# Performance work log

Hardware: AMD Instinct MI355X
Metric: run time of the kernel (lower is better)

Reference implementation:

```python
import jax, jax.numpy as jnp
import numpy as np

B, S, N, H, NH = 2, 2048, 1024, 1024, 16
D = H // NH  # head dim = 64


def setup_inputs() -> dict:
    key = jax.random.key(0)
    ks = jax.random.split(key, 7)
    scale = 1.0 / np.sqrt(H)
    return {
        "token_q": jax.random.normal(ks[0], (B, S, H), dtype=jnp.float32),
        "block_kv": jax.random.normal(ks[1], (B, N, H), dtype=jnp.float32),
        "block_ends": jnp.sort(jax.random.randint(ks[2], (N,), 0, S, dtype=jnp.int32)),
        "Wq": jax.random.normal(ks[3], (H, H), dtype=jnp.float32) * scale,
        "Wk": jax.random.normal(ks[4], (H, H), dtype=jnp.float32) * scale,
        "Wv": jax.random.normal(ks[5], (H, H), dtype=jnp.float32) * scale,
        "Wo": jax.random.normal(ks[6], (H, H), dtype=jnp.float32) * scale,
    }


def reference(token_q, block_kv, block_ends, Wq, Wk, Wv, Wo):
    # nn.Linear: y = x @ W.T (no bias)
    q = (token_q @ Wq.T).reshape(B, S, NH, D).transpose(0, 2, 1, 3)   # [B,h,S,d]
    k = (block_kv @ Wk.T).reshape(B, N, NH, D).transpose(0, 2, 1, 3)  # [B,h,N,d]
    v = (block_kv @ Wv.T).reshape(B, N, NH, D).transpose(0, 2, 1, 3)  # [B,h,N,d]

    attn = jnp.einsum("bhsd,bhnd->bhsn", q, k) / jnp.sqrt(jnp.float32(D))

    # strict_causal mask: block is visible iff its end position <= query index t
    t_idx = jnp.arange(S, dtype=block_ends.dtype)[:, None]           # [S,1]
    mask = block_ends[None, :] <= t_idx                               # [S,N]
    neg = jnp.finfo(attn.dtype).min
    attn = jnp.where(mask[None, None, :, :], attn, neg)

    attn = jax.nn.softmax(attn, axis=-1)
    out = jnp.einsum("bhsn,bhnd->bhsd", attn, v)                      # [B,h,S,d]
    out = out.transpose(0, 2, 1, 3).reshape(B, S, H)
    return out @ Wo.T
```

## Files before the change

### kernel.cpp

```cpp
#include <hip/hip_runtime.h>
#include <float.h>
#include <stdint.h>

#define B_  2
#define S_  2048
#define N_  1024
#define H_  1024
#define NH_ 16
#define K_  1024

typedef __attribute__((ext_vector_type(8))) short bf16x8;
typedef __attribute__((ext_vector_type(4))) float f32x4;

typedef __attribute__((address_space(3))) uint32_t lds_u32;
typedef __attribute__((address_space(1))) uint32_t glb_u32;

__device__ __forceinline__ void gload16(void* l, const void* g) {
    __builtin_amdgcn_global_load_lds((const glb_u32*)g, (lds_u32*)l, 16, 0, 0);
}

__device__ __forceinline__ ushort f2bf(float f) {
    uint32_t u = __float_as_uint(f);
    u = (u + 0x7fffu + ((u >> 16) & 1u)) >> 16;
    return (ushort)u;
}

#if __has_builtin(__builtin_amdgcn_cvt_pk_bf16_f32)
typedef __attribute__((ext_vector_type(2))) __bf16 bfp2;
__device__ __forceinline__ uint pk2(float a, float b) {
    bfp2 v = __builtin_amdgcn_cvt_pk_bf16_f32(a, b);
    return __builtin_bit_cast(uint, v);
}
#else
__device__ __forceinline__ uint pk2(float a, float b) {
    return (uint)f2bf(a) | ((uint)f2bf(b) << 16);
}
#endif

__device__ __forceinline__ float fexp2(float x) {
#if __has_builtin(__builtin_amdgcn_exp2f)
    return __builtin_amdgcn_exp2f(x);
#else
    return exp2f(x);
#endif
}

#define SC2 0.180336880f

__global__ __launch_bounds__(256) void prep_kernel(const float* __restrict__ tq,
        const float* __restrict__ kv, const float* __restrict__ wq,
        const float* __restrict__ wk, const float* __restrict__ wv,
        const float* __restrict__ wo, const int* __restrict__ ends,
        ushort* __restrict__ dst, int* __restrict__ cnt, float* __restrict__ Vm)
{
    int blk = blockIdx.x;
    if (blk >= 5120) {
        if (blk == 5128) {
            float4 z = make_float4(0.f, 0.f, 0.f, 0.f);
            *(float4*)(Vm + threadIdx.x * 8) = z;
            *(float4*)(Vm + threadIdx.x * 8 + 4) = z;
            return;
        }
        int t = (blk - 5120) * 256 + threadIdx.x;
        if (t < S_) {
            int lo = 0, hi = N_;
            while (lo < hi) { int mid = (lo + hi) >> 1; if (ends[mid] <= t) lo = mid + 1; else hi = mid; }
            cnt[t] = lo;
        }
        return;
    }
    const float* src; size_t base;
    if (blk < 2048)      { src = tq; base = 0;       }
    else if (blk < 3072) { src = kv; base = 4194304; blk -= 2048; }
    else if (blk < 3584) { src = wq; base = 6291456; blk -= 3072; }
    else if (blk < 4096) { src = wk; base = 7340032; blk -= 3584; }
    else if (blk < 4608) { src = wv; base = 8388608; blk -= 4096; }
    else                 { src = wo; base = 9437184; blk -= 4608; }
    size_t i = (size_t)blk * 2048 + threadIdx.x * 8;
    float4 a = *(const float4*)(src + i);
    float4 b = *(const float4*)(src + i + 4);
    uint4 o;
    o.x = pk2(a.x, a.y); o.y = pk2(a.z, a.w);
    o.z = pk2(b.x, b.y); o.w = pk2(b.z, b.w);
    *(uint4*)(dst + base + i) = o;
}

__global__ __launch_bounds__(512) void gemm_all(int mode,
        const ushort* __restrict__ qx, const ushort* __restrict__ kvx,
        const ushort* __restrict__ wq, const ushort* __restrict__ wk,
        const ushort* __restrict__ wv, const ushort* __restrict__ wo,
        ushort* __restrict__ Qp, ushort* __restrict__ Kp,
        ushort* __restrict__ VtG, const ushort* __restrict__ AO,
        float* __restrict__ outF, float* __restrict__ Vm)
{
    __shared__ __align__(16) ushort smem[17408];
    ushort* Xs = smem;
    ushort* Ws = smem + 8192;

    const ushort* X; const ushort* W; void* Yp; int kind; float scale = 1.f;
    int bm, bn;
    if (mode == 1) {
        X = AO; W = wo; Yp = outF; kind = 1;
        bm = (blockIdx.x >> 3) * 128; bn = (blockIdx.x & 7) * 128;
    } else {
        int idx = blockIdx.x;
        if (idx < 256)      { X = qx;  W = wq; Yp = Qp;  kind = 0; scale = SC2;
                              bm = (idx >> 3) * 128; bn = (idx & 7) * 128; }
        else if (idx < 384) { int j = idx - 256; X = kvx; W = wk; Yp = Kp; kind = 0;
                              bm = (j >> 3) * 128; bn = (j & 7) * 128; }
        else                { int j = idx - 384; X = kvx; W = wv; Yp = VtG; kind = 2;
                              bm = (j >> 3) * 128; bn = (j & 7) * 128; }
    }

    const int tid = threadIdx.x;
    const int lane = tid & 63, w = tid >> 6;
    const int wy = w >> 1, wx = w & 1;
    const int c = lane & 15, g = lane >> 4;

    f32x4 acc[2][4] = {};

    for (int kt = 0; kt < 16; ++kt) {
        const int k0 = kt * 64;
#pragma unroll
        for (int j = 0; j < 2; ++j) {
            int u = w * 128 + j * 64 + lane;
            int row = u >> 3, gs = (u & 7) ^ (row & 7);
            gload16(Xs + (w * 128 + j * 64) * 8, X + (size_t)(bm + row) * K_ + k0 + gs * 8);
            gload16(Ws + (w * 128 + j * 64) * 8, W + (size_t)(bn + row) * K_ + k0 + gs * 8);
        }
        __syncthreads();
#pragma unroll
        for (int ks = 0; ks < 2; ++ks) {
            bf16x8 af[2], bfr[4];
#pragma unroll
            for (int mi = 0; mi < 2; ++mi) {
                int row = wy * 32 + mi * 16 + c;
                int s = ks * 4 + g;
                af[mi] = *(const bf16x8*)(Xs + (row * 8 + (s ^ (row & 7))) * 8);
            }
#pragma unroll
            for (int ni = 0; ni < 4; ++ni) {
                int row = wx * 64 + ni * 16 + c;
                int s = ks * 4 + g;
                bfr[ni] = *(const bf16x8*)(Ws + (row * 8 + (s ^ (row & 7))) * 8);
            }
#pragma unroll
            for (int mi = 0; mi < 2; ++mi)
#pragma unroll
                for (int ni = 0; ni < 4; ++ni)
                    acc[mi][ni] = __builtin_amdgcn_mfma_f32_16x16x32_bf16(af[mi], bfr[ni], acc[mi][ni], 0, 0, 0);
        }
        __syncthreads();
    }

    if (kind == 0) {
        ushort* Y = (ushort*)Yp;
#pragma unroll
        for (int mi = 0; mi < 2; ++mi)
#pragma unroll
            for (int ni = 0; ni < 4; ++ni)
#pragma unroll
                for (int r = 0; r < 4; ++r) {
                    int row = bm + wy * 32 + mi * 16 + g * 4 + r;
                    int col = bn + wx * 64 + ni * 16 + c;
                    Y[(size_t)row * 1024 + col] = f2bf(acc[mi][ni][r] * scale);
                }
    } else if (kind == 1) {
        float* Y = (float*)Yp;
#pragma unroll
        for (int mi = 0; mi < 2; ++mi)
#pragma unroll
            for (int ni = 0; ni < 4; ++ni)
#pragma unroll
                for (int r = 0; r < 4; ++r) {
                    int row = bm + wy * 32 + mi * 16 + g * 4 + r;
                    int col = bn + wx * 64 + ni * 16 + c;
                    Y[(size_t)row * 1024 + col] = acc[mi][ni][r];
                }
    } else {
        ushort* T = smem;
#pragma unroll
        for (int mi = 0; mi < 2; ++mi)
#pragma unroll
            for (int ni = 0; ni < 4; ++ni) {
                ushort4 v4;
                v4.x = f2bf(acc[mi][ni][0]); v4.y = f2bf(acc[mi][ni][1]);
                v4.z = f2bf(acc[mi][ni][2]); v4.w = f2bf(acc[mi][ni][3]);
                *(ushort4*)&T[(wx * 64 + ni * 16 + c) * 136 + wy * 32 + mi * 16 + g * 4] = v4;
            }
        __syncthreads();
        ushort* Vt = (ushort*)Yp;
        int b = bm >> 10;
        int rid = tid >> 2, quad = tid & 3;
        int n_c = bn + rid;
        int h = n_c >> 6, d = n_c & 63;
        int m0 = quad * 32;
        ushort* dst = Vt + (size_t)((b * NH_ + h) * 64 + d) * N_ + (bm & (N_ - 1)) + m0;
        float vsum = 0.f;
#pragma unroll
        for (int jj = 0; jj < 4; ++jj) {
            uint4 tt = *(const uint4*)&T[rid * 136 + m0 + jj * 8];
            *(uint4*)(dst + jj * 8) = tt;
            uint uu[4] = {tt.x, tt.y, tt.z, tt.w};
#pragma unroll
            for (int q2 = 0; q2 < 4; ++q2) {
                vsum += __uint_as_float(uu[q2] << 16);
                vsum += __uint_as_float(uu[q2] & 0xffff0000u);
            }
        }
        vsum += __shfl_xor(vsum, 1);
        vsum += __shfl_xor(vsum, 2);
        if (quad == 0) atomicAdd(&Vm[b * 1024 + n_c], vsum);
    }
}

__global__ __launch_bounds__(256) void attn_mfma(const ushort* __restrict__ Qp,
                                                 const ushort* __restrict__ Kp,
                                                 const ushort* __restrict__ VtG,
                                                 const int* __restrict__ cnt,
                                                 const float* __restrict__ Vm,
                                                 ushort* __restrict__ AO)
{
    __shared__ __align__(16) ushort Qs[128 * 64];
    __shared__ __align__(16) ushort Ks[64 * 64];
    __shared__ __align__(16) ushort Vs[64 * 64];
    __shared__ __align__(16) ushort Ps[128][72];

    const int id = blockIdx.x;
    const int b = id & 1, h = (id >> 1) & 15;
    const int tb = id >> 5;
    const int t0 = (tb < 8 ? tb : 23 - tb) << 7;
    const int tid = threadIdx.x, lane = tid & 63, w = tid >> 6;
    const int c = lane & 15, g = lane >> 4;

#pragma unroll
    for (int jj = 0; jj < 4; ++jj) {
        int u = w * 256 + jj * 64 + lane;
        int row = u >> 3, gs = (u & 7) ^ (row & 7);
        gload16(Qs + (w * 256 + jj * 64) * 8,
                Qp + (size_t)(b * S_ + t0 + row) * H_ + h * 64 + gs * 8);
    }
    const int cntv0 = cnt[t0 + w * 32 + c];
    const int cntv1 = cnt[t0 + w * 32 + 16 + c];
    const int cnt_min = cnt[t0];
    const int ntmax = (cnt[t0 + 127] + 63) >> 6;

    const int u0 = (w * 2) * 64 + lane, row0 = u0 >> 3, gs0 = (u0 & 7) ^ (row0 & 7);
    const int u1 = (w * 2 + 1) * 64 + lane, row1 = u1 >> 3, gs1 = (u1 & 7) ^ (row1 & 7);
    const ushort* kp0 = Kp + (size_t)(b * N_ + row0) * H_ + h * 64 + gs0 * 8;
    const ushort* kp1 = Kp + (size_t)(b * N_ + row1) * H_ + h * 64 + gs1 * 8;
    const ushort* vp0 = VtG + (size_t)((b * NH_ + h) * 64 + row0) * N_ + gs0 * 8;
    const ushort* vp1 = VtG + (size_t)((b * NH_ + h) * 64 + row1) * N_ + gs1 * 8;

    float l0 = 0.f, l1 = 0.f;
    f32x4 o0[4] = {}, o1[4] = {};

    __syncthreads();
    bf16x8 bq0[2], bq1[2];
#pragma unroll
    for (int ks = 0; ks < 2; ++ks) {
        int s = ks * 4 + g;
        int ra = w * 32 + c;
        bq0[ks] = *(const bf16x8*)(Qs + (ra * 8 + (s ^ (ra & 7))) * 8);
        int rb = w * 32 + 16 + c;
        bq1[ks] = *(const bf16x8*)(Qs + (rb * 8 + (s ^ (rb & 7))) * 8);
    }

    for (int nt = 0; nt < ntmax; ++nt) {
        gload16(Ks + (w * 2) * 512, kp0 + (size_t)nt * 64 * H_);
        gload16(Ks + (w * 2 + 1) * 512, kp1 + (size_t)nt * 64 * H_);
        gload16(Vs + (w * 2) * 512, vp0 + nt * 64);
        gload16(Vs + (w * 2 + 1) * 512, vp1 + nt * 64);
        __syncthreads();

        f32x4 st0[4] = {}, st1[4] = {};
#pragma unroll
        for (int ntile = 0; ntile < 4; ++ntile)
#pragma unroll
            for (int ks = 0; ks < 2; ++ks) {
                int row = ntile * 16 + c;
                int s = ks * 4 + g;
                bf16x8 ak = *(const bf16x8*)(Ks + (row * 8 + (s ^ (row & 7))) * 8);
                st0[ntile] = __builtin_amdgcn_mfma_f32_16x16x32_bf16(ak, bq0[ks], st0[ntile], 0, 0, 0);
                st1[ntile] = __builtin_amdgcn_mfma_f32_16x16x32_bf16(ak, bq1[ks], st1[ntile], 0, 0, 0);
            }

        const bool full = ((nt + 1) << 6) <= cnt_min;
        float lsum0 = 0.f, lsum1 = 0.f;
        if (full) {
#pragma unroll
            for (int ntile = 0; ntile < 4; ++ntile) {
                float a0 = fexp2(st0[ntile][0]), a1 = fexp2(st0[ntile][1]);
                float a2 = fexp2(st0[ntile][2]), a3 = fexp2(st0[ntile][3]);
                lsum0 += (a0 + a1) + (a2 + a3);
                uint2 pw; pw.x = pk2(a0, a1); pw.y = pk2(a2, a3);
                *(uint2*)&Ps[w * 32 + c][ntile * 16 + g * 4] = pw;
                float b0 = fexp2(st1[ntile][0]), b1 = fexp2(st1[ntile][1]);
                float b2 = fexp2(st1[ntile][2]), b3 = fexp2(st1[ntile][3]);
                lsum1 += (b0 + b1) + (b2 + b3);
                uint2 qw; qw.x = pk2(b0, b1); qw.y = pk2(b2, b3);
                *(uint2*)&Ps[w * 32 + 16 + c][ntile * 16 + g * 4] = qw;
            }
        } else {
            const int base0 = (nt << 6) + g * 4 - cntv0;
            const int base1 = (nt << 6) + g * 4 - cntv1;
#pragma unroll
            for (int ntile = 0; ntile < 4; ++ntile) {
                float a0 = (base0 + ntile * 16 + 0 >= 0) ? 0.f : fexp2(st0[ntile][0]);
                float a1 = (base0 + ntile * 16 + 1 >= 0) ? 0.f : fexp2(st0[ntile][1]);
                float a2 = (base0 + ntile * 16 + 2 >= 0) ? 0.f : fexp2(st0[ntile][2]);
                float a3 = (base0 + ntile * 16 + 3 >= 0) ? 0.f : fexp2(st0[ntile][3]);
                lsum0 += (a0 + a1) + (a2 + a3);
                uint2 pw; pw.x = pk2(a0, a1); pw.y = pk2(a2, a3);
                *(uint2*)&Ps[w * 32 + c][ntile * 16 + g * 4] = pw;
                float b0 = (base1 + ntile * 16 + 0 >= 0) ? 0.f : fexp2(st1[ntile][0]);
                float b1 = (base1 + ntile * 16 + 1 >= 0) ? 0.f : fexp2(st1[ntile][1]);
                float b2 = (base1 + ntile * 16 + 2 >= 0) ? 0.f : fexp2(st1[ntile][2]);
                float b3 = (base1 + ntile * 16 + 3 >= 0) ? 0.f : fexp2(st1[ntile][3]);
                lsum1 += (b0 + b1) + (b2 + b3);
                uint2 qw; qw.x = pk2(b0, b1); qw.y = pk2(b2, b3);
                *(uint2*)&Ps[w * 32 + 16 + c][ntile * 16 + g * 4] = qw;
            }
        }
        lsum0 += __shfl_xor(lsum0, 16); lsum0 += __shfl_xor(lsum0, 32);
        lsum1 += __shfl_xor(lsum1, 16); lsum1 += __shfl_xor(lsum1, 32);
        l0 += lsum0; l1 += lsum1;

        bf16x8 ap0[2], ap1[2];
#pragma unroll
        for (int ks = 0; ks < 2; ++ks) {
            ap0[ks] = *(const bf16x8*)&Ps[w * 32 + c][ks * 32 + g * 8];
            ap1[ks] = *(const bf16x8*)&Ps[w * 32 + 16 + c][ks * 32 + g * 8];
        }
#pragma unroll
        for (int dt = 0; dt < 4; ++dt)
#pragma unroll
            for (int ks = 0; ks < 2; ++ks) {
                int row = dt * 16 + c;
                int s = ks * 4 + g;
                bf16x8 bv = *(const bf16x8*)(Vs + (row * 8 + (s ^ (row & 7))) * 8);
                o0[dt] = __builtin_amdgcn_mfma_f32_16x16x32_bf16(ap0[ks], bv, o0[dt], 0, 0, 0);
                o1[dt] = __builtin_amdgcn_mfma_f32_16x16x32_bf16(ap1[ks], bv, o1[dt], 0, 0, 0);
            }
        __syncthreads();
    }

#pragma unroll
    for (int qt = 0; qt < 2; ++qt) {
        float invl = 1.f / (qt == 0 ? l0 : l1);
        f32x4* o = (qt == 0 ? o0 : o1);
        float lr[4]; int cq[4];
#pragma unroll
        for (int r = 0; r < 4; ++r) {
            lr[r] = __shfl(invl, g * 4 + r);
            cq[r] = cnt[t0 + w * 32 + qt * 16 + g * 4 + r];
        }
#pragma unroll
        for (int dt = 0; dt < 4; ++dt)
#pragma unroll
            for (int r = 0; r < 4; ++r) {
                int q = t0 + w * 32 + qt * 16 + g * 4 + r;
                float val = o[dt][r] * lr[r];
                if (cq[r] == 0) val = Vm[b * 1024 + h * 64 + dt * 16 + c] * (1.f / 1024.f);
                AO[(size_t)(b * S_ + q) * H_ + h * 64 + dt * 16 + c] = f2bf(val);
            }
    }
}

extern "C" void kernel_launch(void* const* d_in, const int* in_sizes, int n_in,
                              void* d_out, int out_size, void* d_ws, size_t ws_size,
                              hipStream_t stream) {
    const float* token_q    = (const float*)d_in[0];
    const float* block_kv   = (const float*)d_in[1];
    const int*   block_ends = (const int*)d_in[2];
    const float* Wq = (const float*)d_in[3];
    const float* Wk = (const float*)d_in[4];
    const float* Wv = (const float*)d_in[5];
    const float* Wo = (const float*)d_in[6];
    float* out = (float*)d_out;

    ushort* ws  = (ushort*)d_ws;
    ushort* qx  = ws;
    ushort* kvx = ws + (size_t)4 * 1024 * 1024;
    ushort* wqb = ws + (size_t)6 * 1024 * 1024;
    ushort* wkb = ws + (size_t)7 * 1024 * 1024;
    ushort* wvb = ws + (size_t)8 * 1024 * 1024;
    ushort* wob = ws + (size_t)9 * 1024 * 1024;
    ushort* Qp  = ws + (size_t)10 * 1024 * 1024;
    ushort* Kp  = ws + (size_t)14 * 1024 * 1024;
    ushort* VtG = ws + (size_t)16 * 1024 * 1024;
    int*    cnt = (int*)(ws + (size_t)18 * 1024 * 1024);
    float*  Vm  = (float*)(ws + (size_t)18 * 1024 * 1024 + 4096);

    prep_kernel<<<5129, 256, 0, stream>>>(token_q, block_kv, Wq, Wk, Wv, Wo,
                                          block_ends, ws, cnt, Vm);
    gemm_all<<<512, 512, 0, stream>>>(0, qx, kvx, wqb, wkb, wvb, wob,
                                      Qp, Kp, VtG, nullptr, nullptr, Vm);
    attn_mfma<<<512, 256, 0, stream>>>(Qp, Kp, VtG, cnt, Vm, Qp);
    gemm_all<<<256, 512, 0, stream>>>(1, qx, kvx, wqb, wkb, wvb, wob,
                                      Qp, Kp, VtG, Qp, out, Vm);
}
```

Baseline: 163.0 us.

## Fuse fp32-to-bf16 conversion into GEMM loads and drop the prep kernel

```diff
diff --git a/kernel.cpp b/kernel.cpp
--- a/kernel.cpp
+++ b/kernel.cpp
@@ -47,68 +47,30 @@
 
 #define SC2 0.180336880f
 
-__global__ __launch_bounds__(256) void prep_kernel(const float* __restrict__ tq,
-        const float* __restrict__ kv, const float* __restrict__ wq,
-        const float* __restrict__ wk, const float* __restrict__ wv,
-        const float* __restrict__ wo, const int* __restrict__ ends,
-        ushort* __restrict__ dst, int* __restrict__ cnt, float* __restrict__ Vm)
-{
-    int blk = blockIdx.x;
-    if (blk >= 5120) {
-        if (blk == 5128) {
-            float4 z = make_float4(0.f, 0.f, 0.f, 0.f);
-            *(float4*)(Vm + threadIdx.x * 8) = z;
-            *(float4*)(Vm + threadIdx.x * 8 + 4) = z;
-            return;
-        }
-        int t = (blk - 5120) * 256 + threadIdx.x;
-        if (t < S_) {
-            int lo = 0, hi = N_;
-            while (lo < hi) { int mid = (lo + hi) >> 1; if (ends[mid] <= t) lo = mid + 1; else hi = mid; }
-            cnt[t] = lo;
-        }
-        return;
-    }
-    const float* src; size_t base;
-    if (blk < 2048)      { src = tq; base = 0;       }
-    else if (blk < 3072) { src = kv; base = 4194304; blk -= 2048; }
-    else if (blk < 3584) { src = wq; base = 6291456; blk -= 3072; }
-    else if (blk < 4096) { src = wk; base = 7340032; blk -= 3584; }
-    else if (blk < 4608) { src = wv; base = 8388608; blk -= 4096; }
-    else                 { src = wo; base = 9437184; blk -= 4608; }
-    size_t i = (size_t)blk * 2048 + threadIdx.x * 8;
-    float4 a = *(const float4*)(src + i);
-    float4 b = *(const float4*)(src + i + 4);
-    uint4 o;
-    o.x = pk2(a.x, a.y); o.y = pk2(a.z, a.w);
-    o.z = pk2(b.x, b.y); o.w = pk2(b.z, b.w);
-    *(uint4*)(dst + base + i) = o;
-}
-
 __global__ __launch_bounds__(512) void gemm_all(int mode,
-        const ushort* __restrict__ qx, const ushort* __restrict__ kvx,
-        const ushort* __restrict__ wq, const ushort* __restrict__ wk,
-        const ushort* __restrict__ wv, const ushort* __restrict__ wo,
+        const float* __restrict__ tqF, const float* __restrict__ kvF,
+        const float* __restrict__ wqF, const float* __restrict__ wkF,
+        const float* __restrict__ wvF, const float* __restrict__ woF,
         ushort* __restrict__ Qp, ushort* __restrict__ Kp,
         ushort* __restrict__ VtG, const ushort* __restrict__ AO,
-        float* __restrict__ outF, float* __restrict__ Vm)
+        float* __restrict__ outF, float* __restrict__ VmP)
 {
     __shared__ __align__(16) ushort smem[17408];
     ushort* Xs = smem;
     ushort* Ws = smem + 8192;
 
-    const ushort* X; const ushort* W; void* Yp; int kind; float scale = 1.f;
+    const float* XF = nullptr; const float* WF; void* Yp; int kind; float scale = 1.f;
     int bm, bn;
     if (mode == 1) {
-        X = AO; W = wo; Yp = outF; kind = 1;
+        WF = woF; Yp = outF; kind = 1;
         bm = (blockIdx.x >> 3) * 128; bn = (blockIdx.x & 7) * 128;
     } else {
         int idx = blockIdx.x;
-        if (idx < 256)      { X = qx;  W = wq; Yp = Qp;  kind = 0; scale = SC2;
+        if (idx < 256)      { XF = tqF; WF = wqF; Yp = Qp;  kind = 0; scale = SC2;
                               bm = (idx >> 3) * 128; bn = (idx & 7) * 128; }
-        else if (idx < 384) { int j = idx - 256; X = kvx; W = wk; Yp = Kp; kind = 0;
+        else if (idx < 384) { int j = idx - 256; XF = kvF; WF = wkF; Yp = Kp; kind = 0;
                               bm = (j >> 3) * 128; bn = (j & 7) * 128; }
-        else                { int j = idx - 384; X = kvx; W = wv; Yp = VtG; kind = 2;
+        else                { int j = idx - 384; XF = kvF; WF = wvF; Yp = VtG; kind = 2;
                               bm = (j >> 3) * 128; bn = (j & 7) * 128; }
     }
 
@@ -117,18 +79,63 @@
     const int wy = w >> 1, wx = w & 1;
     const int c = lane & 15, g = lane >> 4;
 
+    const int u0 = w * 128 + lane,      row0 = u0 >> 3, gs0 = (u0 & 7) ^ (row0 & 7);
+    const int u1 = w * 128 + 64 + lane, row1 = u1 >> 3, gs1 = (u1 & 7) ^ (row1 & 7);
+
+    const ushort* xb0 = nullptr; const ushort* xb1 = nullptr;
+    const float *xs0 = nullptr, *xs1 = nullptr;
+    if (mode == 1) {
+        xb0 = AO + (size_t)(bm + row0) * K_ + gs0 * 8;
+        xb1 = AO + (size_t)(bm + row1) * K_ + gs1 * 8;
+    } else {
+        xs0 = XF + (size_t)(bm + row0) * K_ + gs0 * 8;
+        xs1 = XF + (size_t)(bm + row1) * K_ + gs1 * 8;
+    }
+    const float* ws0 = WF + (size_t)(bn + row0) * K_ + gs0 * 8;
+    const float* ws1 = WF + (size_t)(bn + row1) * K_ + gs1 * 8;
+
+    float4 x0a, x0b, x1a, x1b, w0a, w0b, w1a, w1b;
+    uint4 bx0, bx1;
+
+    auto loadX = [&](int k0) {
+        if (mode == 1) {
+            bx0 = *(const uint4*)(xb0 + k0);
+            bx1 = *(const uint4*)(xb1 + k0);
+        } else {
+            x0a = *(const float4*)(xs0 + k0); x0b = *(const float4*)(xs0 + k0 + 4);
+            x1a = *(const float4*)(xs1 + k0); x1b = *(const float4*)(xs1 + k0 + 4);
+        }
+        w0a = *(const float4*)(ws0 + k0); w0b = *(const float4*)(ws0 + k0 + 4);
+        w1a = *(const float4*)(ws1 + k0); w1b = *(const float4*)(ws1 + k0 + 4);
+    };
+
     f32x4 acc[2][4] = {};
 
+    loadX(0);
     for (int kt = 0; kt < 16; ++kt) {
-        const int k0 = kt * 64;
-#pragma unroll
-        for (int j = 0; j < 2; ++j) {
-            int u = w * 128 + j * 64 + lane;
-            int row = u >> 3, gs = (u & 7) ^ (row & 7);
-            gload16(Xs + (w * 128 + j * 64) * 8, X + (size_t)(bm + row) * K_ + k0 + gs * 8);
-            gload16(Ws + (w * 128 + j * 64) * 8, W + (size_t)(bn + row) * K_ + k0 + gs * 8);
-        }
-        __syncthreads();
+        __syncthreads();
+        if (mode == 1) {
+            *(uint4*)(Xs + u0 * 8) = bx0;
+            *(uint4*)(Xs + u1 * 8) = bx1;
+        } else {
+            uint4 t0v = make_uint4(pk2(x0a.x, x0a.y), pk2(x0a.z, x0a.w),
+                                   pk2(x0b.x, x0b.y), pk2(x0b.z, x0b.w));
+            uint4 t1v = make_uint4(pk2(x1a.x, x1a.y), pk2(x1a.z, x1a.w),
+                                   pk2(x1b.x, x1b.y), pk2(x1b.z, x1b.w));
+            *(uint4*)(Xs + u0 * 8) = t0v;
+            *(uint4*)(Xs + u1 * 8) = t1v;
+        }
+        {
+            uint4 s0 = make_uint4(pk2(w0a.x, w0a.y), pk2(w0a.z, w0a.w),
+                                  pk2(w0b.x, w0b.y), pk2(w0b.z, w0b.w));
+            uint4 s1 = make_uint4(pk2(w1a.x, w1a.y), pk2(w1a.z, w1a.w),
+                                  pk2(w1b.x, w1b.y), pk2(w1b.z, w1b.w));
+            *(uint4*)(Ws + u0 * 8) = s0;
+            *(uint4*)(Ws + u1 * 8) = s1;
+        }
+        __syncthreads();
+        if (kt < 15) loadX((kt + 1) * 64);
+
 #pragma unroll
         for (int ks = 0; ks < 2; ++ks) {
             bf16x8 af[2], bfr[4];
@@ -150,7 +157,6 @@
                 for (int ni = 0; ni < 4; ++ni)
                     acc[mi][ni] = __builtin_amdgcn_mfma_f32_16x16x32_bf16(af[mi], bfr[ni], acc[mi][ni], 0, 0, 0);
         }
-        __syncthreads();
     }
 
     if (kind == 0) {
@@ -179,6 +185,7 @@
                 }
     } else {
         ushort* T = smem;
+        __syncthreads();
 #pragma unroll
         for (int mi = 0; mi < 2; ++mi)
 #pragma unroll
@@ -210,21 +217,22 @@
         }
         vsum += __shfl_xor(vsum, 1);
         vsum += __shfl_xor(vsum, 2);
-        if (quad == 0) atomicAdd(&Vm[b * 1024 + n_c], vsum);
+        if (quad == 0) VmP[(bm >> 7) * 1024 + n_c] = vsum;
     }
 }
 
 __global__ __launch_bounds__(256) void attn_mfma(const ushort* __restrict__ Qp,
                                                  const ushort* __restrict__ Kp,
                                                  const ushort* __restrict__ VtG,
-                                                 const int* __restrict__ cnt,
-                                                 const float* __restrict__ Vm,
+                                                 const int* __restrict__ ends,
+                                                 const float* __restrict__ VmP,
                                                  ushort* __restrict__ AO)
 {
     __shared__ __align__(16) ushort Qs[128 * 64];
     __shared__ __align__(16) ushort Ks[64 * 64];
     __shared__ __align__(16) ushort Vs[64 * 64];
     __shared__ __align__(16) ushort Ps[128][72];
+    __shared__ int cntS[128];
 
     const int id = blockIdx.x;
     const int b = id & 1, h = (id >> 1) & 15;
@@ -240,10 +248,12 @@
         gload16(Qs + (w * 256 + jj * 64) * 8,
                 Qp + (size_t)(b * S_ + t0 + row) * H_ + h * 64 + gs * 8);
     }
-    const int cntv0 = cnt[t0 + w * 32 + c];
-    const int cntv1 = cnt[t0 + w * 32 + 16 + c];
-    const int cnt_min = cnt[t0];
-    const int ntmax = (cnt[t0 + 127] + 63) >> 6;
+    if (tid < 128) {
+        int t = t0 + tid;
+        int lo = 0, hi = N_;
+        while (lo < hi) { int mid = (lo + hi) >> 1; if (ends[mid] <= t) lo = mid + 1; else hi = mid; }
+        cntS[tid] = lo;
+    }
 
     const int u0 = (w * 2) * 64 + lane, row0 = u0 >> 3, gs0 = (u0 & 7) ^ (row0 & 7);
     const int u1 = (w * 2 + 1) * 64 + lane, row1 = u1 >> 3, gs1 = (u1 & 7) ^ (row1 & 7);
@@ -256,6 +266,11 @@
     f32x4 o0[4] = {}, o1[4] = {};
 
     __syncthreads();
+    const int cntv0 = cntS[w * 32 + c];
+    const int cntv1 = cntS[w * 32 + 16 + c];
+    const int cnt_min = cntS[0];
+    const int ntmax = (cntS[127] + 63) >> 6;
+
     bf16x8 bq0[2], bq1[2];
 #pragma unroll
     for (int ks = 0; ks < 2; ++ks) {
@@ -353,7 +368,7 @@
 #pragma unroll
         for (int r = 0; r < 4; ++r) {
             lr[r] = __shfl(invl, g * 4 + r);
-            cq[r] = cnt[t0 + w * 32 + qt * 16 + g * 4 + r];
+            cq[r] = cntS[w * 32 + qt * 16 + g * 4 + r];
         }
 #pragma unroll
         for (int dt = 0; dt < 4; ++dt)
@@ -361,7 +376,13 @@
             for (int r = 0; r < 4; ++r) {
                 int q = t0 + w * 32 + qt * 16 + g * 4 + r;
                 float val = o[dt][r] * lr[r];
-                if (cq[r] == 0) val = Vm[b * 1024 + h * 64 + dt * 16 + c] * (1.f / 1024.f);
+                if (cq[r] == 0) {
+                    float sm = 0.f;
+#pragma unroll
+                    for (int j = 0; j < 8; ++j)
+                        sm += VmP[(b * 8 + j) * 1024 + h * 64 + dt * 16 + c];
+                    val = sm * (1.f / 1024.f);
+                }
                 AO[(size_t)(b * S_ + q) * H_ + h * 64 + dt * 16 + c] = f2bf(val);
             }
     }
@@ -380,23 +401,14 @@
     float* out = (float*)d_out;
 
     ushort* ws  = (ushort*)d_ws;
-    ushort* qx  = ws;
-    ushort* kvx = ws + (size_t)4 * 1024 * 1024;
-    ushort* wqb = ws + (size_t)6 * 1024 * 1024;
-    ushort* wkb = ws + (size_t)7 * 1024 * 1024;
-    ushort* wvb = ws + (size_t)8 * 1024 * 1024;
-    ushort* wob = ws + (size_t)9 * 1024 * 1024;
-    ushort* Qp  = ws + (size_t)10 * 1024 * 1024;
-    ushort* Kp  = ws + (size_t)14 * 1024 * 1024;
-    ushort* VtG = ws + (size_t)16 * 1024 * 1024;
-    int*    cnt = (int*)(ws + (size_t)18 * 1024 * 1024);
-    float*  Vm  = (float*)(ws + (size_t)18 * 1024 * 1024 + 4096);
-
-    prep_kernel<<<5129, 256, 0, stream>>>(token_q, block_kv, Wq, Wk, Wv, Wo,
-                                          block_ends, ws, cnt, Vm);
-    gemm_all<<<512, 512, 0, stream>>>(0, qx, kvx, wqb, wkb, wvb, wob,
-                                      Qp, Kp, VtG, nullptr, nullptr, Vm);
-    attn_mfma<<<512, 256, 0, stream>>>(Qp, Kp, VtG, cnt, Vm, Qp);
-    gemm_all<<<256, 512, 0, stream>>>(1, qx, kvx, wqb, wkb, wvb, wob,
-                                      Qp, Kp, VtG, Qp, out, Vm);
-}
+    ushort* Qp  = ws;
+    ushort* Kp  = ws + (size_t)4 * 1024 * 1024;
+    ushort* VtG = ws + (size_t)6 * 1024 * 1024;
+    float*  VmP = (float*)(ws + (size_t)8 * 1024 * 1024);
+
+    gemm_all<<<512, 512, 0, stream>>>(0, token_q, block_kv, Wq, Wk, Wv, Wo,
+                                      Qp, Kp, VtG, nullptr, nullptr, VmP);
+    attn_mfma<<<512, 256, 0, stream>>>(Qp, Kp, VtG, block_ends, VmP, Qp);
+    gemm_all<<<256, 512, 0, stream>>>(1, token_q, block_kv, Wq, Wk, Wv, Wo,
+                                      Qp, Kp, VtG, Qp, out, VmP);
+}
```

Measured after the change: 205.6 us. 26.1% more time.

## Split out-projection into smaller-tile GEMM, move count search into attention

Applied to the files above, without the earlier changes.

```diff
diff --git a/kernel.cpp b/kernel.cpp
--- a/kernel.cpp
+++ b/kernel.cpp
@@ -50,25 +50,9 @@
 __global__ __launch_bounds__(256) void prep_kernel(const float* __restrict__ tq,
         const float* __restrict__ kv, const float* __restrict__ wq,
         const float* __restrict__ wk, const float* __restrict__ wv,
-        const float* __restrict__ wo, const int* __restrict__ ends,
-        ushort* __restrict__ dst, int* __restrict__ cnt, float* __restrict__ Vm)
+        const float* __restrict__ wo, ushort* __restrict__ dst)
 {
     int blk = blockIdx.x;
-    if (blk >= 5120) {
-        if (blk == 5128) {
-            float4 z = make_float4(0.f, 0.f, 0.f, 0.f);
-            *(float4*)(Vm + threadIdx.x * 8) = z;
-            *(float4*)(Vm + threadIdx.x * 8 + 4) = z;
-            return;
-        }
-        int t = (blk - 5120) * 256 + threadIdx.x;
-        if (t < S_) {
-            int lo = 0, hi = N_;
-            while (lo < hi) { int mid = (lo + hi) >> 1; if (ends[mid] <= t) lo = mid + 1; else hi = mid; }
-            cnt[t] = lo;
-        }
-        return;
-    }
     const float* src; size_t base;
     if (blk < 2048)      { src = tq; base = 0;       }
     else if (blk < 3072) { src = kv; base = 4194304; blk -= 2048; }
@@ -85,13 +69,12 @@
     *(uint4*)(dst + base + i) = o;
 }
 
-__global__ __launch_bounds__(512) void gemm_all(int mode,
+__global__ __launch_bounds__(512) void gemm_qkv(
         const ushort* __restrict__ qx, const ushort* __restrict__ kvx,
         const ushort* __restrict__ wq, const ushort* __restrict__ wk,
-        const ushort* __restrict__ wv, const ushort* __restrict__ wo,
+        const ushort* __restrict__ wv,
         ushort* __restrict__ Qp, ushort* __restrict__ Kp,
-        ushort* __restrict__ VtG, const ushort* __restrict__ AO,
-        float* __restrict__ outF, float* __restrict__ Vm)
+        ushort* __restrict__ VtG, float* __restrict__ VmP)
 {
     __shared__ __align__(16) ushort smem[17408];
     ushort* Xs = smem;
@@ -99,10 +82,7 @@
 
     const ushort* X; const ushort* W; void* Yp; int kind; float scale = 1.f;
     int bm, bn;
-    if (mode == 1) {
-        X = AO; W = wo; Yp = outF; kind = 1;
-        bm = (blockIdx.x >> 3) * 128; bn = (blockIdx.x & 7) * 128;
-    } else {
+    {
         int idx = blockIdx.x;
         if (idx < 256)      { X = qx;  W = wq; Yp = Qp;  kind = 0; scale = SC2;
                               bm = (idx >> 3) * 128; bn = (idx & 7) * 128; }
@@ -164,18 +144,6 @@
                     int row = bm + wy * 32 + mi * 16 + g * 4 + r;
                     int col = bn + wx * 64 + ni * 16 + c;
                     Y[(size_t)row * 1024 + col] = f2bf(acc[mi][ni][r] * scale);
-                }
-    } else if (kind == 1) {
-        float* Y = (float*)Yp;
-#pragma unroll
-        for (int mi = 0; mi < 2; ++mi)
-#pragma unroll
-            for (int ni = 0; ni < 4; ++ni)
-#pragma unroll
-                for (int r = 0; r < 4; ++r) {
-                    int row = bm + wy * 32 + mi * 16 + g * 4 + r;
-                    int col = bn + wx * 64 + ni * 16 + c;
-                    Y[(size_t)row * 1024 + col] = acc[mi][ni][r];
                 }
     } else {
         ushort* T = smem;
@@ -210,21 +178,22 @@
         }
         vsum += __shfl_xor(vsum, 1);
         vsum += __shfl_xor(vsum, 2);
-        if (quad == 0) atomicAdd(&Vm[b * 1024 + n_c], vsum);
+        if (quad == 0) VmP[(bm >> 7) * 1024 + n_c] = vsum;
     }
 }
 
 __global__ __launch_bounds__(256) void attn_mfma(const ushort* __restrict__ Qp,
                                                  const ushort* __restrict__ Kp,
                                                  const ushort* __restrict__ VtG,
-                                                 const int* __restrict__ cnt,
-                                                 const float* __restrict__ Vm,
+                                                 const int* __restrict__ ends,
+                                                 const float* __restrict__ VmP,
                                                  ushort* __restrict__ AO)
 {
     __shared__ __align__(16) ushort Qs[128 * 64];
     __shared__ __align__(16) ushort Ks[64 * 64];
     __shared__ __align__(16) ushort Vs[64 * 64];
     __shared__ __align__(16) ushort Ps[128][72];
+    __shared__ int cntS[128];
 
     const int id = blockIdx.x;
     const int b = id & 1, h = (id >> 1) & 15;
@@ -240,10 +209,12 @@
         gload16(Qs + (w * 256 + jj * 64) * 8,
                 Qp + (size_t)(b * S_ + t0 + row) * H_ + h * 64 + gs * 8);
     }
-    const int cntv0 = cnt[t0 + w * 32 + c];
-    const int cntv1 = cnt[t0 + w * 32 + 16 + c];
-    const int cnt_min = cnt[t0];
-    const int ntmax = (cnt[t0 + 127] + 63) >> 6;
+    if (tid < 128) {
+        int t = t0 + tid;
+        int lo = 0, hi = N_;
+        while (lo < hi) { int mid = (lo + hi) >> 1; if (ends[mid] <= t) lo = mid + 1; else hi = mid; }
+        cntS[tid] = lo;
+    }
 
     const int u0 = (w * 2) * 64 + lane, row0 = u0 >> 3, gs0 = (u0 & 7) ^ (row0 & 7);
     const int u1 = (w * 2 + 1) * 64 + lane, row1 = u1 >> 3, gs1 = (u1 & 7) ^ (row1 & 7);
@@ -256,6 +227,11 @@
     f32x4 o0[4] = {}, o1[4] = {};
 
     __syncthreads();
+    const int cntv0 = cntS[w * 32 + c];
+    const int cntv1 = cntS[w * 32 + 16 + c];
+    const int cnt_min = cntS[0];
+    const int ntmax = (cntS[127] + 63) >> 6;
+
     bf16x8 bq0[2], bq1[2];
 #pragma unroll
     for (int ks = 0; ks < 2; ++ks) {
@@ -353,7 +329,7 @@
 #pragma unroll
         for (int r = 0; r < 4; ++r) {
             lr[r] = __shfl(invl, g * 4 + r);
-            cq[r] = cnt[t0 + w * 32 + qt * 16 + g * 4 + r];
+            cq[r] = cntS[w * 32 + qt * 16 + g * 4 + r];
         }
 #pragma unroll
         for (int dt = 0; dt < 4; ++dt)
@@ -361,10 +337,81 @@
             for (int r = 0; r < 4; ++r) {
                 int q = t0 + w * 32 + qt * 16 + g * 4 + r;
                 float val = o[dt][r] * lr[r];
-                if (cq[r] == 0) val = Vm[b * 1024 + h * 64 + dt * 16 + c] * (1.f / 1024.f);
+                if (cq[r] == 0) {
+                    float sm = 0.f;
+#pragma unroll
+                    for (int j = 0; j < 8; ++j)
+                        sm += VmP[(b * 8 + j) * 1024 + h * 64 + dt * 16 + c];
+                    val = sm * (1.f / 1024.f);
+                }
                 AO[(size_t)(b * S_ + q) * H_ + h * 64 + dt * 16 + c] = f2bf(val);
             }
     }
+}
+
+__global__ __launch_bounds__(512) void gemm_out(const ushort* __restrict__ AO,
+                                                const ushort* __restrict__ wo,
+                                                float* __restrict__ out)
+{
+    __shared__ __align__(16) ushort Xs[64 * 64];
+    __shared__ __align__(16) ushort Ws[128 * 64];
+
+    const int bm = (blockIdx.x >> 3) * 64;
+    const int bn = (blockIdx.x & 7) * 128;
+    const int tid = threadIdx.x, lane = tid & 63, w = tid >> 6;
+    const int wy = w >> 2, wx = w & 3;
+    const int c = lane & 15, g = lane >> 4;
+
+    const int rx = tid >> 3,          sx = (tid & 7) ^ (rx & 7);
+    const int rw0 = tid >> 3,         sw0 = (tid & 7) ^ (rw0 & 7);
+    const int uw1 = tid + 512;
+    const int rw1 = uw1 >> 3,         sw1 = (uw1 & 7) ^ (rw1 & 7);
+
+    const ushort* xp  = AO + (size_t)(bm + rx) * K_ + sx * 8;
+    const ushort* wp0 = wo + (size_t)(bn + rw0) * K_ + sw0 * 8;
+    const ushort* wp1 = wo + (size_t)(bn + rw1) * K_ + sw1 * 8;
+
+    f32x4 acc[2][2] = {};
+
+    for (int kt = 0; kt < 16; ++kt) {
+        const int k0 = kt * 64;
+        gload16(Xs + (w * 64) * 8, xp + k0);
+        gload16(Ws + (w * 64) * 8, wp0 + k0);
+        gload16(Ws + (512 + w * 64) * 8, wp1 + k0);
+        __syncthreads();
+#pragma unroll
+        for (int ks = 0; ks < 2; ++ks) {
+            bf16x8 af[2], bfr[2];
+            int s = ks * 4 + g;
+#pragma unroll
+            for (int mi = 0; mi < 2; ++mi) {
+                int row = wy * 32 + mi * 16 + c;
+                af[mi] = *(const bf16x8*)(Xs + (row * 8 + (s ^ (row & 7))) * 8);
+            }
+#pragma unroll
+            for (int ni = 0; ni < 2; ++ni) {
+                int row = wx * 32 + ni * 16 + c;
+                bfr[ni] = *(const bf16x8*)(Ws + (row * 8 + (s ^ (row & 7))) * 8);
+            }
+#pragma unroll
+            for (int mi = 0; mi < 2; ++mi)
+#pragma unroll
+                for (int ni = 0; ni < 2; ++ni)
+                    acc[mi][ni] = __builtin_amdgcn_mfma_f32_16x16x32_bf16(af[mi], bfr[ni], acc[mi][ni], 0, 0, 0);
+        }
+        __syncthreads();
+    }
+
+#pragma unroll
+    for (int mi = 0; mi < 2; ++mi)
+#pragma unroll
+        for (int ni = 0; ni < 2; ++ni)
+#pragma unroll
+            for (int r = 0; r < 4; ++r) {
+                int row = bm + wy * 32 + mi * 16 + g * 4 + r;
+                int col = bn + wx * 32 + ni * 16 + c;
+                out[(size_t)row * 1024 + col] = acc[mi][ni][r];
+            }
 }
 
 extern "C" void kernel_launch(void* const* d_in, const int* in_sizes, int n_in,
@@ -389,14 +436,10 @@
     ushort* Qp  = ws + (size_t)10 * 1024 * 1024;
     ushort* Kp  = ws + (size_t)14 * 1024 * 1024;
     ushort* VtG = ws + (size_t)16 * 1024 * 1024;
-    int*    cnt = (int*)(ws + (size_t)18 * 1024 * 1024);
-    float*  Vm  = (float*)(ws + (size_t)18 * 1024 * 1024 + 4096);
-
-    prep_kernel<<<5129, 256, 0, stream>>>(token_q, block_kv, Wq, Wk, Wv, Wo,
-                                          block_ends, ws, cnt, Vm);
-    gemm_all<<<512, 512, 0, stream>>>(0, qx, kvx, wqb, wkb, wvb, wob,
-                                      Qp, Kp, VtG, nullptr, nullptr, Vm);
-    attn_mfma<<<512, 256, 0, stream>>>(Qp, Kp, VtG, cnt, Vm, Qp);
-    gemm_all<<<256, 512, 0, stream>>>(1, qx, kvx, wqb, wkb, wvb, wob,
-                                      Qp, Kp, VtG, Qp, out, Vm);
-}
+    float*  VmP = (float*)(ws + (size_t)18 * 1024 * 1024);
+
+    prep_kernel<<<5120, 256, 0, stream>>>(token_q, block_kv, Wq, Wk, Wv, Wo, ws);
+    gemm_qkv<<<512, 512, 0, stream>>>(qx, kvx, wqb, wkb, wvb, Qp, Kp, VtG, VmP);
+    attn_mfma<<<512, 256, 0, stream>>>(Qp, Kp, VtG, block_ends, VmP, Qp);
+    gemm_out<<<512, 512, 0, stream>>>(Qp, wob, out);
+}
```

Measured after the change: 159.1 us. 1.02x faster.
